# Kernel tuning notes

Measured on AMD Instinct MI355X. Metric: run time of the kernel, lower is better.

The kernel has to match this reference:

```python
import jax, jax.numpy as jnp
import numpy as np

SIDELEN = 128
PIXEL_SZ = 1.0
PI = float(np.pi)
CHUNK = 128  # atoms per scan step; keeps per-step intermediate ~170 MB


def setup_inputs() -> dict:
    key = jax.random.key(0)
    k1, k2, k3 = jax.random.split(key, 3)
    coords = jax.random.normal(k1, (4, 2048, 3), dtype=jnp.float32) * 10.0  # angstrom-ish spread
    # form factors must be positive (ff_b appears as 4*pi/ff_b); keep away from 0
    ff_a = jax.random.uniform(k2, (2048, 5), dtype=jnp.float32, minval=0.5, maxval=2.0)
    ff_b = jax.random.uniform(k3, (2048, 5), dtype=jnp.float32, minval=0.5, maxval=2.0)
    return {"coords": coords, "ff_a": ff_a, "ff_b": ff_b}


def _grid_2d():
    ax = jnp.arange(-(SIDELEN // 2), (SIDELEN - 1) // 2 + 1, dtype=jnp.float32)
    X, Y = jnp.meshgrid(ax, ax, indexing="ij")  # torch.meshgrid default is 'ij'
    return jnp.stack([Y, X], axis=-1).reshape(-1, 2) * PIXEL_SZ  # [P, 2]


def _potential(coords2d, ff_a, ff_b, grid):
    # coords2d: [B, A, 2]; ff_a, ff_b: [A, 5]; grid: [P, 2]
    B, A, _ = coords2d.shape
    P = grid.shape[0]
    invb = (4.0 * PI) / ff_b                      # [A, 5]
    coef = ff_a * invb                            # [A, 5]
    nc = A // CHUNK
    ac = coords2d.reshape(B, nc, CHUNK, 2).transpose(1, 0, 2, 3)  # [nc, B, C, 2]
    ib = invb.reshape(nc, CHUNK, 5)
    cc = coef.reshape(nc, CHUNK, 5)

    def step(acc, chunk):
        a, ibc, ccc = chunk
        diff = grid[None, None, :, :] - a[:, :, None, :]          # [B, C, P, 2]
        d2 = jnp.sum(diff * diff, axis=-1)                        # [B, C, P]
        # dist_sq = invb * ||dx||^2 per form factor; contrib = exp(-pi*dist_sq)*ff_a*invb
        e = jnp.exp(-PI * ib_bcast(ibc) * d2[:, :, None, :])      # [B, C, 5, P]
        acc = acc + jnp.einsum("bcfp,cf->bp", e, ccc)
        return acc, None

    def ib_bcast(ibc):
        return ibc[None, :, :, None]  # [1, C, 5, 1]

    acc0 = jnp.zeros((B, P), dtype=coords2d.dtype)
    pot, _ = jax.lax.scan(step, acc0, (ac, ib, cc))
    return pot  # [B, P]


def reference(coords, ff_a, ff_b):
    B = coords.shape[0]
    grid = _grid_2d()
    pot = _potential(coords[..., :2], ff_a, ff_b, grid)
    return pot.reshape(B, 1, SIDELEN, SIDELEN)
```

## Files before the change

kernel.cpp:

```cpp
#include <hip/hip_runtime.h>

#define SIDE 128
#define PI_F 3.14159265358979f
#define RMAX 1.4f
#define BLK 512

__global__ void __launch_bounds__(BLK) potential_stripe(
        const float* __restrict__ coords,
        const float* __restrict__ ff_a,
        const float* __restrict__ ff_b,
        float* __restrict__ out,
        int A) {
    const int s    = blockIdx.x;
    const int b    = blockIdx.y;
    const int row0 = s * 2;
    const int t    = threadIdx.x;
    const int lane = t & 63;

    __shared__ float img[2 * SIDE];
    __shared__ int   cnt;
    __shared__ float lx[2048], ly[2048];
    __shared__ int   li[2048];

    if (t < 2 * SIDE) img[t] = 0.0f;
    if (t == 0) cnt = 0;
    __syncthreads();

    const float* cb = coords + (size_t)b * A * 3;

    const float ylo = (float)row0 - RMAX;
    const float yhi = (float)(row0 + 1) + RMAX;
    for (int a0 = 0; a0 < A; a0 += BLK) {
        int a = a0 + t;
        float cx = 0.f, cy = 0.f;
        bool keep = false;
        if (a < A) {
            cx = cb[a * 3 + 0] + 64.0f;
            cy = cb[a * 3 + 1] + 64.0f;
            keep = (cy >= ylo) & (cy <= yhi) &
                   (cx >= -RMAX) & (cx <= 127.0f + RMAX);
        }
        unsigned long long m = __ballot(keep);
        int nw  = __popcll(m);
        int pos = __popcll(m & ((1ull << lane) - 1ull));
        int base = 0;
        if (lane == 0 && nw) base = atomicAdd(&cnt, nw);
        base = __shfl(base, 0);
        if (keep) {
            int k = base + pos;
            lx[k] = cx; ly[k] = cy; li[k] = a;
        }
    }
    __syncthreads();

    const int n = cnt;
    for (int k = t; k < n; k += BLK) {
        float cx = lx[k];
        float cy = ly[k];
        int   a  = li[k];
        #pragma unroll
        for (int f = 0; f < 5; ++f) {
            float fa = ff_a[a * 5 + f];
            float fb = ff_b[a * 5 + f];
            float invb = (4.0f * PI_F) / fb;
            float coef = fa * invb;
            float c    = PI_F * invb;
            float r = sqrtf((__logf(coef) + 32.0f) / c);

            int i0 = max(row0,     (int)ceilf(cy - r));
            int i1 = min(row0 + 1, (int)floorf(cy + r));
            int j0 = max(0,        (int)ceilf(cx - r));
            int j1 = min(SIDE - 1, (int)floorf(cx + r));

            for (int i = i0; i <= i1; ++i) {
                float dy  = (float)i - cy;
                float wyi = coef * __expf(-c * dy * dy);
                float* rowp = img + (i - row0) * SIDE;
                for (int j = j0; j <= j1; ++j) {
                    float dx = (float)j - cx;
                    atomicAdd(&rowp[j], wyi * __expf(-c * dx * dx));
                }
            }
        }
    }
    __syncthreads();

    if (t < (2 * SIDE) / 4) {
        float4* ov = (float4*)(out + ((size_t)b * SIDE + row0) * SIDE);
        ov[t] = ((const float4*)img)[t];
    }
}

extern "C" void kernel_launch(void* const* d_in, const int* in_sizes, int n_in,
                              void* d_out, int out_size, void* d_ws, size_t ws_size,
                              hipStream_t stream) {
    const float* coords = (const float*)d_in[0];
    const float* ffa    = (const float*)d_in[1];
    const float* ffb    = (const float*)d_in[2];
    float* out = (float*)d_out;

    int A = in_sizes[1] / 5;
    int B = in_sizes[0] / (A * 3);

    dim3 grid(SIDE / 2, B);
    potential_stripe<<<grid, BLK, 0, stream>>>(coords, ffa, ffb, out, A);
}
```

Measured before the change: 63.80 us.

## Process one row per block and drop shared atom compaction

Each block now handles a single image row instead of two, which doubles the block count. Atoms are filtered and splatted directly in the load loop instead of being compacted into shared-memory lists first. The per-form-factor cutoff radius (log/sqrt) is replaced by the fixed RMAX window, so fewer instructions run per atom. In exchange, every block rereads all coordinates, divergence across kept and rejected atoms goes up, and the fixed window may evaluate more pixels than the adaptive radius did.

```diff
diff --git a/kernel.cpp b/kernel.cpp
--- a/kernel.cpp
+++ b/kernel.cpp
@@ -5,88 +5,54 @@
 #define RMAX 1.4f
 #define BLK 512
 
-__global__ void __launch_bounds__(BLK) potential_stripe(
+__global__ void __launch_bounds__(BLK) potential_row(
         const float* __restrict__ coords,
         const float* __restrict__ ff_a,
         const float* __restrict__ ff_b,
         float* __restrict__ out,
         int A) {
-    const int s    = blockIdx.x;
-    const int b    = blockIdx.y;
-    const int row0 = s * 2;
-    const int t    = threadIdx.x;
-    const int lane = t & 63;
+    const int row = blockIdx.x;
+    const int b   = blockIdx.y;
+    const int t   = threadIdx.x;
 
-    __shared__ float img[2 * SIDE];
-    __shared__ int   cnt;
-    __shared__ float lx[2048], ly[2048];
-    __shared__ int   li[2048];
-
-    if (t < 2 * SIDE) img[t] = 0.0f;
-    if (t == 0) cnt = 0;
+    __shared__ float img[SIDE];
+    if (t < SIDE) img[t] = 0.0f;
     __syncthreads();
 
-    const float* cb = coords + (size_t)b * A * 3;
+    const float* cb  = coords + (size_t)b * A * 3;
+    const float  ylo = (float)row - RMAX;
+    const float  yhi = (float)row + RMAX;
 
-    const float ylo = (float)row0 - RMAX;
-    const float yhi = (float)(row0 + 1) + RMAX;
-    for (int a0 = 0; a0 < A; a0 += BLK) {
-        int a = a0 + t;
-        float cx = 0.f, cy = 0.f;
-        bool keep = false;
-        if (a < A) {
-            cx = cb[a * 3 + 0] + 64.0f;
-            cy = cb[a * 3 + 1] + 64.0f;
-            keep = (cy >= ylo) & (cy <= yhi) &
-                   (cx >= -RMAX) & (cx <= 127.0f + RMAX);
-        }
-        unsigned long long m = __ballot(keep);
-        int nw  = __popcll(m);
-        int pos = __popcll(m & ((1ull << lane) - 1ull));
-        int base = 0;
-        if (lane == 0 && nw) base = atomicAdd(&cnt, nw);
-        base = __shfl(base, 0);
-        if (keep) {
-            int k = base + pos;
-            lx[k] = cx; ly[k] = cy; li[k] = a;
-        }
-    }
-    __syncthreads();
+    for (int a = t; a < A; a += BLK) {
+        const float cx = cb[a * 3 + 0] + 64.0f;
+        const float cy = cb[a * 3 + 1] + 64.0f;
+        const bool keep = (cy >= ylo) & (cy <= yhi) &
+                          (cx >= -RMAX) & (cx <= 127.0f + RMAX);
+        if (!keep) continue;
 
-    const int n = cnt;
-    for (int k = t; k < n; k += BLK) {
-        float cx = lx[k];
-        float cy = ly[k];
-        int   a  = li[k];
+        const float dy  = (float)row - cy;
+        const float dy2 = dy * dy;
+        const int j0 = max(0,        (int)ceilf(cx - RMAX));
+        const int j1 = min(SIDE - 1, (int)floorf(cx + RMAX));
+
+        const float* fa = ff_a + a * 5;
+        const float* fb = ff_b + a * 5;
         #pragma unroll
         for (int f = 0; f < 5; ++f) {
-            float fa = ff_a[a * 5 + f];
-            float fb = ff_b[a * 5 + f];
-            float invb = (4.0f * PI_F) / fb;
-            float coef = fa * invb;
-            float c    = PI_F * invb;
-            float r = sqrtf((__logf(coef) + 32.0f) / c);
-
-            int i0 = max(row0,     (int)ceilf(cy - r));
-            int i1 = min(row0 + 1, (int)floorf(cy + r));
-            int j0 = max(0,        (int)ceilf(cx - r));
-            int j1 = min(SIDE - 1, (int)floorf(cx + r));
-
-            for (int i = i0; i <= i1; ++i) {
-                float dy  = (float)i - cy;
-                float wyi = coef * __expf(-c * dy * dy);
-                float* rowp = img + (i - row0) * SIDE;
-                for (int j = j0; j <= j1; ++j) {
-                    float dx = (float)j - cx;
-                    atomicAdd(&rowp[j], wyi * __expf(-c * dx * dx));
-                }
+            const float invb = (4.0f * PI_F) / fb[f];
+            const float coef = fa[f] * invb;
+            const float c    = PI_F * invb;
+            const float wyi  = coef * __expf(-c * dy2);
+            for (int j = j0; j <= j1; ++j) {
+                const float dx = (float)j - cx;
+                atomicAdd(&img[j], wyi * __expf(-c * dx * dx));
             }
         }
     }
     __syncthreads();
 
-    if (t < (2 * SIDE) / 4) {
-        float4* ov = (float4*)(out + ((size_t)b * SIDE + row0) * SIDE);
+    if (t < SIDE / 4) {
+        float4* ov = (float4*)(out + ((size_t)b * SIDE + row) * SIDE);
         ov[t] = ((const float4*)img)[t];
     }
 }
@@ -102,6 +68,6 @@
     int A = in_sizes[1] / 5;
     int B = in_sizes[0] / (A * 3);
 
-    dim3 grid(SIDE / 2, B);
-    potential_stripe<<<grid, BLK, 0, stream>>>(coords, ffa, ffb, out, A);
+    dim3 grid(SIDE, B);
+    potential_row<<<grid, BLK, 0, stream>>>(coords, ffa, ffb, out, A);
 }
```

Measured after the change: 68.43 us. 1.07x slower.
